# Performance work log

Hardware: AMD Instinct MI355X
Metric: run time of the kernel (lower is better)

Reference implementation:

```python
import jax, jax.numpy as jnp
import numpy as np

N, E, D, T, R, H = 100000, 800000, 128, 4, 4, 8
DK = D // H
LN_EPS = 1e-5


def _per_type_proj(x, W, b, node_type):
    # x:[N,D], W:[T,D,D], b:[T,D] -> select projection by each node's type
    proj = jnp.einsum('ni,tio->nto', x, W) + b[None]          # [N,T,D]
    return jnp.take_along_axis(proj, node_type[:, None, None], axis=1)[:, 0]  # [N,D]


def setup_inputs() -> dict:
    key = jax.random.key(0)
    ks = jax.random.split(key, 12)
    sW = 1.0 / np.sqrt(D)
    sR = np.sqrt(2.0 / (DK + DK))  # glorot for [dk,dk]
    return {
        'x': jax.random.normal(ks[0], (N, D), jnp.float32),
        'node_type': jax.random.randint(ks[1], (N,), 0, T, jnp.int32),
        'edge_index': jax.random.randint(ks[2], (2, E), 0, N, jnp.int32),
        'edge_type': jax.random.randint(ks[3], (E,), 0, R, jnp.int32),
        'edge_spatial': jnp.zeros((E,), jnp.int32),
        'Wk': jax.random.normal(ks[4], (T, D, D), jnp.float32) * sW,
        'bk': jnp.zeros((T, D), jnp.float32),
        'Wq': jax.random.normal(ks[5], (T, D, D), jnp.float32) * sW,
        'bq': jnp.zeros((T, D), jnp.float32),
        'Wv': jax.random.normal(ks[6], (T, D, D), jnp.float32) * sW,
        'bv': jnp.zeros((T, D), jnp.float32),
        'Wa': jax.random.normal(ks[7], (T, D, D), jnp.float32) * sW,
        'ba': jnp.zeros((T, D), jnp.float32),
        'rel_pri': jnp.ones((R, H), jnp.float32),
        'rel_att': jax.random.normal(ks[8], (R, H, DK, DK), jnp.float32) * sR,
        'rel_msg': jax.random.normal(ks[9], (R, H, DK, DK), jnp.float32) * sR,
        'skip': jnp.ones((T,), jnp.float32),
        'ln_gamma': jnp.ones((T, D), jnp.float32),
        'ln_beta': jnp.zeros((T, D), jnp.float32),
    }


def reference(x, node_type, edge_index, edge_type, edge_spatial,
              Wk, bk, Wq, bq, Wv, bv, Wa, ba,
              rel_pri, rel_att, rel_msg, skip, ln_gamma, ln_beta):
    src, dst = edge_index[0], edge_index[1]  # PyG: row0 = source j, row1 = target i

    # per-type linear projections, selected by node type
    K = _per_type_proj(x, Wk, bk, node_type)
    Q = _per_type_proj(x, Wq, bq, node_type)
    V = _per_type_proj(x, Wv, bv, node_type)

    q_e = Q[dst].reshape(E, H, DK)
    k_e = K[src].reshape(E, H, DK)
    v_e = V[src].reshape(E, H, DK)

    # per-relation transforms without materializing [E,H,DK,DK] gathers
    k_rel = jnp.zeros_like(k_e)
    msg = jnp.zeros_like(v_e)
    for r in range(R):
        m = (edge_type == r)[:, None, None]
        k_rel = k_rel + jnp.where(m, jnp.einsum('ehd,hdk->ehk', k_e, rel_att[r]), 0.0)
        msg = msg + jnp.where(m, jnp.einsum('ehd,hdk->ehk', v_e, rel_msg[r]), 0.0)

    logits = (q_e * k_rel).sum(-1) * rel_pri[edge_type] / np.sqrt(DK)  # [E,H]

    # segment softmax over destination nodes
    seg_max = jax.ops.segment_max(logits, dst, num_segments=N)
    seg_max = jnp.where(jnp.isfinite(seg_max), seg_max, 0.0)
    ex = jnp.exp(logits - seg_max[dst])
    denom = jax.ops.segment_sum(ex, dst, num_segments=N)
    att = ex / denom[dst]  # [E,H]

    aggr = jax.ops.segment_sum(msg * att[:, :, None], dst, num_segments=N)  # [N,H,DK]
    h = jax.nn.gelu(aggr.reshape(N, D), approximate=False)

    trans = _per_type_proj(h, Wa, ba, node_type)
    alpha = jax.nn.sigmoid(skip)[node_type][:, None]
    pre = trans * alpha + x * (1.0 - alpha)

    # per-type LayerNorm
    mu = pre.mean(-1, keepdims=True)
    var = ((pre - mu) ** 2).mean(-1, keepdims=True)
    norm = (pre - mu) * jax.lax.rsqrt(var + LN_EPS)
    return norm * ln_gamma[node_type] + ln_beta[node_type]
```

## Files before the change

kernel.cpp:

```cpp
#include <hip/hip_runtime.h>
#include <math.h>

#define D_DIM 128

using bf16x8 = __attribute__((ext_vector_type(8))) short;
using f32x4  = __attribute__((ext_vector_type(4))) float;

__device__ __forceinline__ unsigned short f2bf(float f) {
    unsigned u = __float_as_uint(f);
    u += 0x7fffu + ((u >> 16) & 1u);
    return (unsigned short)(u >> 16);
}

__global__ __launch_bounds__(256)
void count_types_k(const int* __restrict__ nt, int* __restrict__ blockcnt, int N) {
    __shared__ int wcnt[4][4];
    int tid = threadIdx.x;
    int i = blockIdx.x * 256 + tid;
    int w = tid >> 6, l = tid & 63;
    int t = (i < N) ? nt[i] : -1;
    #pragma unroll
    for (int tt = 0; tt < 4; ++tt) {
        unsigned long long m = __ballot(t == tt);
        if (l == 0) wcnt[w][tt] = __popcll(m);
    }
    __syncthreads();
    if (tid < 4) {
        blockcnt[blockIdx.x * 4 + tid] =
            wcnt[0][tid] + wcnt[1][tid] + wcnt[2][tid] + wcnt[3][tid];
    }
}

__global__ __launch_bounds__(256)
void scan_blocks_k(const int* __restrict__ blockcnt, int nb,
                   int* __restrict__ boff, int* __restrict__ pad_off) {
    __shared__ int tot_s[4];
    __shared__ int po_s[5];
    int tid = threadIdx.x;
    int t = tid >> 6, l = tid & 63;
    int sum = 0;
    for (int base = 0; base < nb; base += 64) {
        int b = base + l;
        sum += (b < nb) ? blockcnt[b * 4 + t] : 0;
    }
    #pragma unroll
    for (int m = 1; m < 64; m <<= 1) sum += __shfl_xor(sum, m);
    if (l == 0) tot_s[t] = sum;
    __syncthreads();
    if (tid == 0) {
        int s = 0;
        for (int tt = 0; tt < 4; ++tt) { po_s[tt] = s; s += ((tot_s[tt] + 63) >> 6) << 6; }
        po_s[4] = s;
        for (int tt = 0; tt < 5; ++tt) pad_off[tt] = po_s[tt];
    }
    __syncthreads();
    int run = po_s[t];
    for (int base = 0; base < nb; base += 64) {
        int b = base + l;
        int v = (b < nb) ? blockcnt[b * 4 + t] : 0;
        int incl = v;
        #pragma unroll
        for (int off = 1; off < 64; off <<= 1) {
            int up = __shfl_up(incl, off);
            if (l >= off) incl += up;
        }
        if (b < nb) boff[b * 4 + t] = run + incl - v;
        run += __shfl(incl, 63);
    }
}

__global__ __launch_bounds__(256)
void scatter_types_k(const int* __restrict__ nt, const int* __restrict__ boff,
                     int* __restrict__ order_p, int N) {
    __shared__ int wbase[4][4];
    int tid = threadIdx.x;
    int i = blockIdx.x * 256 + tid;
    int w = tid >> 6, l = tid & 63;
    int t = (i < N) ? nt[i] : -1;
    int rank = 0;
    #pragma unroll
    for (int tt = 0; tt < 4; ++tt) {
        unsigned long long m = __ballot(t == tt);
        if (l == 0) wbase[w][tt] = __popcll(m);
        if (t == tt) rank = __popcll(m & ((1ull << l) - 1ull));
    }
    __syncthreads();
    if (tid < 4) {
        int run = 0;
        for (int ww = 0; ww < 4; ++ww) { int c = wbase[ww][tid]; wbase[ww][tid] = run; run += c; }
    }
    __syncthreads();
    if (i < N) order_p[boff[blockIdx.x * 4 + t] + wbase[w][t] + rank] = i;
}

__global__ void convw_k(const float* __restrict__ Wq, const float* __restrict__ Wa,
                        unsigned short* __restrict__ Wqt, unsigned short* __restrict__ Wat) {
    int i = blockIdx.x * 256 + threadIdx.x;
    int t = i >> 14, rem = i & 16383, row = rem >> 7, col = rem & 127;
    int d = (t << 14) | (col << 7) | row;
    Wqt[d] = f2bf(Wq[i]);
    Wat[d] = f2bf(Wa[i]);
}

__global__ void combine_kr_k(const float* __restrict__ Wk, const float* __restrict__ rel_att,
                             const float* __restrict__ rel_pri,
                             unsigned short* __restrict__ W_kr_t) {
    int idx = blockIdx.x * 256 + threadIdx.x;
    int i = idx & 127;
    int col = (idx >> 7) & 127;
    int r = (idx >> 14) & 3;
    int t = idx >> 16;
    int h = col >> 4, k = col & 15;
    const float* wk = Wk + t * 16384 + i * 128 + h * 16;
    const float* ra = rel_att + ((r * 8 + h) * 16) * 16 + k;
    float s = 0.f;
    #pragma unroll
    for (int d = 0; d < 16; ++d) s += wk[d] * ra[d * 16];
    W_kr_t[idx] = f2bf(s * rel_pri[r * 8 + h] * 0.25f);
}
__global__ void combine_bkr_k(const float* __restrict__ bk, const float* __restrict__ rel_att,
                              const float* __restrict__ rel_pri, float* __restrict__ bkr) {
    int idx = blockIdx.x * 256 + threadIdx.x;
    if (idx >= 2048) return;
    int col = idx & 127;
    int r = (idx >> 7) & 3;
    int t = idx >> 9;
    int h = col >> 4, k = col & 15;
    float s = 0.f;
    #pragma unroll
    for (int d = 0; d < 16; ++d)
        s += bk[t * 128 + h * 16 + d] * rel_att[((r * 8 + h) * 16 + d) * 16 + k];
    bkr[idx] = s * rel_pri[r * 8 + h] * 0.25f;
}

__global__ void combine_vm_k(const float* __restrict__ Wv, const float* __restrict__ rel_msg,
                             unsigned short* __restrict__ W_vm_t) {
    int idx = blockIdx.x * 256 + threadIdx.x;
    int i = idx & 127;
    int col = (idx >> 7) & 127;
    int r = (idx >> 14) & 3;
    int t = idx >> 16;
    int h = col >> 4, k = col & 15;
    const float* wv = Wv + t * 16384 + i * 128 + h * 16;
    const float* rm = rel_msg + ((r * 8 + h) * 16) * 16 + k;
    float s = 0.f;
    #pragma unroll
    for (int d = 0; d < 16; ++d) s += wv[d] * rm[d * 16];
    W_vm_t[idx] = f2bf(s);
}
__global__ void combine_bvm_k(const float* __restrict__ bv, const float* __restrict__ rel_msg,
                              float* __restrict__ bvm) {
    int idx = blockIdx.x * 256 + threadIdx.x;
    if (idx >= 2048) return;
    int col = idx & 127;
    int r = (idx >> 7) & 3;
    int t = idx >> 9;
    int h = col >> 4, k = col & 15;
    float s = 0.f;
    #pragma unroll
    for (int d = 0; d < 16; ++d)
        s += bv[t * 128 + h * 16 + d] * rel_msg[((r * 8 + h) * 16 + d) * 16 + k];
    bvm[idx] = s;
}

__global__ void deg_k(const int* __restrict__ ei, int* __restrict__ deg, int E) {
    int e = blockIdx.x * 256 + threadIdx.x;
    if (e < E) atomicAdd(&deg[ei[E + e]], 1);
}
__global__ void scan1_k(const int* __restrict__ deg, int* __restrict__ excl,
                        int* __restrict__ bsum, int N) {
    __shared__ int s[512];
    int i = blockIdx.x * 512 + threadIdx.x;
    int v = (i < N) ? deg[i] : 0;
    s[threadIdx.x] = v;
    __syncthreads();
    for (int off = 1; off < 512; off <<= 1) {
        int t = (threadIdx.x >= off) ? s[threadIdx.x - off] : 0;
        __syncthreads();
        s[threadIdx.x] += t;
        __syncthreads();
    }
    if (i < N) excl[i] = s[threadIdx.x] - v;
    if (threadIdx.x == 511) bsum[blockIdx.x] = s[511];
}
__global__ void scan2_k(int* __restrict__ bsum, int nb) {
    int l = threadIdx.x & 63;
    int run = 0;
    for (int base = 0; base < nb; base += 64) {
        int b = base + l;
        int v = (b < nb) ? bsum[b] : 0;
        int incl = v;
        #pragma unroll
        for (int off = 1; off < 64; off <<= 1) {
            int up = __shfl_up(incl, off);
            if (l >= off) incl += up;
        }
        if (b < nb) bsum[b] = run + incl - v;
        run += __shfl(incl, 63);
    }
}
__global__ void scan3_k(int* __restrict__ excl, const int* __restrict__ bsum, int N) {
    int i = blockIdx.x * 512 + threadIdx.x;
    if (i < N) excl[i] += bsum[blockIdx.x];
}
__global__ void scatter_edges_k(const int* __restrict__ ei, const int* __restrict__ et,
                                const int* __restrict__ off, int* __restrict__ cursor,
                                int* __restrict__ elist, int E) {
    int e = blockIdx.x * 256 + threadIdx.x;
    if (e < E) {
        int dst = ei[E + e];
        int p = off[dst] + atomicAdd(&cursor[dst], 1);
        elist[p] = (ei[e] << 2) | et[e];
    }
}

__global__ __launch_bounds__(256, 4)
void proj_mfma(const float* __restrict__ x, const int* __restrict__ order_p,
               const int* __restrict__ pad_off,
               const unsigned short* __restrict__ Wqt, const float* __restrict__ bq,
               const unsigned short* __restrict__ W_kr_t, const float* __restrict__ bkr,
               const unsigned short* __restrict__ W_vm_t, const float* __restrict__ bvm,
               unsigned short* __restrict__ Qb, unsigned short* __restrict__ KRb,
               unsigned short* __restrict__ VMb, int N) {
    __shared__ unsigned shmem[64 * 128];
    __shared__ int gid_s[64];
    unsigned* xs = shmem;
    char* stageb = (char*)shmem;
    int tid = threadIdx.x;
    int base = blockIdx.x * 64;
    int t = (base >= pad_off[1]) + (base >= pad_off[2]) + (base >= pad_off[3]);

    if (tid < 64) gid_s[tid] = order_p[base + tid];
    __syncthreads();

    {
        int row = tid >> 2, q = tid & 3;
        int g = gid_s[row];
        const float4* xr = (const float4*)(x + (size_t)(g < 0 ? 0 : g) * 128 + q * 32);
        int swz = (row & 7) << 4;
        #pragma unroll
        for (int v4 = 0; v4 < 8; ++v4) {
            float4 f = (g >= 0) ? xr[v4] : make_float4(0.f, 0.f, 0.f, 0.f);
            unsigned ua = (unsigned)f2bf(f.x) | ((unsigned)f2bf(f.y) << 16);
            unsigned ub = (unsigned)f2bf(f.z) | ((unsigned)f2bf(f.w) << 16);
            int c2 = (q * 16 + v4 * 2) * 4;
            xs[(row << 6) + (((c2) ^ swz) >> 2)] = ua;
            xs[(row << 6) + (((c2 + 4) ^ swz) >> 2)] = ub;
        }
    }
    __syncthreads();

    int w = tid >> 6, l = tid & 63;
    int lr = l & 15, lg = l >> 4;

    bf16x8 afr[4][4];
    #pragma unroll
    for (int j = 0; j < 4; ++j) {
        int row = j * 16 + lr;
        #pragma unroll
        for (int ks = 0; ks < 4; ++ks) {
            int byteoff = (ks * 64 + lg * 16) ^ ((lr & 7) << 4);
            afr[j][ks] = *reinterpret_cast<const bf16x8*>(
                reinterpret_cast<const char*>(&xs[row << 6]) + byteoff);
        }
    }
    __syncthreads();

    #pragma unroll 1
    for (int pass = 0; pass < 4; ++pass) {
        int m0 = (pass & 1) * 2;
        const unsigned short* Wp;
        const float* bp;
        unsigned short* dstp;
        if (pass < 2) { Wp = W_kr_t; bp = bkr; dstp = KRb; }
        else          { Wp = W_vm_t; bp = bvm; dstp = VMb; }
        Wp += (size_t)(t * 4 + m0) << 14;
        bp += (t * 4 + m0) * 128;

        #pragma unroll
        for (int ci = 0; ci < 2; ++ci) {
            int c = w * 2 + ci;
            #pragma unroll
            for (int mm = 0; mm < 2; ++mm) {
                const unsigned short* wb = Wp + ((size_t)mm << 14)
                                         + (size_t)(c * 16 + lr) * 128 + lg * 8;
                bf16x8 wfr[4];
                #pragma unroll
                for (int ks = 0; ks < 4; ++ks) wfr[ks] = *(const bf16x8*)(wb + ks * 32);
                f32x4 acc0 = {0.f,0.f,0.f,0.f}, acc1 = {0.f,0.f,0.f,0.f};
                f32x4 acc2 = {0.f,0.f,0.f,0.f}, acc3 = {0.f,0.f,0.f,0.f};
                #pragma unroll
                for (int ks = 0; ks < 4; ++ks) {
                    acc0 = __builtin_amdgcn_mfma_f32_16x16x32_bf16(wfr[ks], afr[0][ks], acc0, 0, 0, 0);
                    acc1 = __builtin_amdgcn_mfma_f32_16x16x32_bf16(wfr[ks], afr[1][ks], acc1, 0, 0, 0);
                    acc2 = __builtin_amdgcn_mfma_f32_16x16x32_bf16(wfr[ks], afr[2][ks], acc2, 0, 0, 0);
                    acc3 = __builtin_amdgcn_mfma_f32_16x16x32_bf16(wfr[ks], afr[3][ks], acc3, 0, 0, 0);
                }
                float4 bb = *(const float4*)&bp[mm * 128 + c * 16 + lg * 4];
                int colb = (mm * 128 + c * 16 + lg * 4) * 2;
                f32x4 accs[4] = {acc0, acc1, acc2, acc3};
                #pragma unroll
                for (int j = 0; j < 4; ++j) {
                    int node = j * 16 + lr;
                    unsigned p0 = (unsigned)f2bf(accs[j][0] + bb.x) | ((unsigned)f2bf(accs[j][1] + bb.y) << 16);
                    unsigned p1 = (unsigned)f2bf(accs[j][2] + bb.z) | ((unsigned)f2bf(accs[j][3] + bb.w) << 16);
                    int byte = (node * 512 + colb) ^ ((node & 7) << 4);
                    *(uint2*)(stageb + byte) = make_uint2(p0, p1);
                }
            }
        }
        __syncthreads();
        #pragma unroll
        for (int i = 0; i < 8; ++i) {
            int row = w * 16 + i * 2 + (l >> 5);
            int l32 = l & 31;
            int byte = (row * 512 + l32 * 16) ^ ((row & 7) << 4);
            uint4 v = *(const uint4*)(stageb + byte);
            int g = gid_s[row];
            if (g >= 0)
                *(uint4*)&dstp[(size_t)g * 512 + (pass & 1) * 256 + l32 * 8] = v;
        }
        __syncthreads();
    }

    #pragma unroll
    for (int ci = 0; ci < 2; ++ci) {
        int c = w * 2 + ci;
        const unsigned short* wb = Wqt + ((size_t)t << 14) + (size_t)(c * 16 + lr) * 128 + lg * 8;
        bf16x8 wfr[4];
        #pragma unroll
        for (int ks = 0; ks < 4; ++ks) wfr[ks] = *(const bf16x8*)(wb + ks * 32);
        f32x4 acc0 = {0.f,0.f,0.f,0.f}, acc1 = {0.f,0.f,0.f,0.f};
        f32x4 acc2 = {0.f,0.f,0.f,0.f}, acc3 = {0.f,0.f,0.f,0.f};
        #pragma unroll
        for (int ks = 0; ks < 4; ++ks) {
            acc0 = __builtin_amdgcn_mfma_f32_16x16x32_bf16(wfr[ks], afr[0][ks], acc0, 0, 0, 0);
            acc1 = __builtin_amdgcn_mfma_f32_16x16x32_bf16(wfr[ks], afr[1][ks], acc1, 0, 0, 0);
            acc2 = __builtin_amdgcn_mfma_f32_16x16x32_bf16(wfr[ks], afr[2][ks], acc2, 0, 0, 0);
            acc3 = __builtin_amdgcn_mfma_f32_16x16x32_bf16(wfr[ks], afr[3][ks], acc3, 0, 0, 0);
        }
        float4 bb = *(const float4*)&bq[t * 128 + c * 16 + lg * 4];
        int colb = (c * 16 + lg * 4) * 2;
        f32x4 accs[4] = {acc0, acc1, acc2, acc3};
        #pragma unroll
        for (int j = 0; j < 4; ++j) {
            int node = j * 16 + lr;
            unsigned p0 = (unsigned)f2bf(accs[j][0] + bb.x) | ((unsigned)f2bf(accs[j][1] + bb.y) << 16);
            unsigned p1 = (unsigned)f2bf(accs[j][2] + bb.z) | ((unsigned)f2bf(accs[j][3] + bb.w) << 16);
            int byte = (node * 256 + colb) ^ ((node & 7) << 4);
            *(uint2*)(stageb + byte) = make_uint2(p0, p1);
        }
    }
    __syncthreads();
    #pragma unroll
    for (int i = 0; i < 4; ++i) {
        int row = w * 16 + i * 4 + (l >> 4);
        int l16 = l & 15;
        int byte = (row * 256 + l16 * 16) ^ ((row & 7) << 4);
        uint4 v = *(const uint4*)(stageb + byte);
        int g = gid_s[row];
        if (g >= 0) *(uint4*)&Qb[(size_t)g * 128 + l16 * 8] = v;
    }
}

__global__ __launch_bounds__(256)
void edge_fused(const unsigned short* __restrict__ Qb,
                const unsigned short* __restrict__ KRb,
                const unsigned short* __restrict__ VMb,
                const int* __restrict__ off, const int* __restrict__ elist,
                float* __restrict__ aggr, int N, int E) {
    int w = threadIdx.x >> 6, l = threadIdx.x & 63;
    int dst = blockIdx.x * 4 + w;
    if (dst >= N) return;
    int q = l >> 4, c = l & 15;

    float Qf[8];
    {
        bf16x8 qv = *(const bf16x8*)&Qb[(size_t)dst * 128 + c * 8];
        const unsigned* qu = (const unsigned*)&qv;
        #pragma unroll
        for (int i = 0; i < 4; ++i) {
            Qf[2 * i]     = __uint_as_float(qu[i] << 16);
            Qf[2 * i + 1] = __uint_as_float(qu[i] & 0xffff0000u);
        }
    }

    float S[8] = {0.f, 0.f, 0.f, 0.f, 0.f, 0.f, 0.f, 0.f};
    float den = 0.f;

    int e0 = off[dst];
    int e1 = (dst == N - 1) ? E : off[dst + 1];
    int deg = e1 - e0;

    for (int base = 0; base < deg; base += 64) {
        int cnt = min(64, deg - base);
        int pk_l = elist[e0 + min(base + l, deg - 1)];
        for (int s = 0; s < cnt; s += 8) {
            int eA = min(s + q, cnt - 1);
            int eB = min(s + 4 + q, cnt - 1);
            int pkA = __shfl(pk_l, eA);
            int pkB = __shfl(pk_l, eB);
            bf16x8 krA = *(const bf16x8*)&KRb[(size_t)pkA * 128 + c * 8];
            bf16x8 krB = *(const bf16x8*)&KRb[(size_t)pkB * 128 + c * 8];
            bf16x8 vmA = *(const bf16x8*)&VMb[(size_t)pkA * 128 + c * 8];
            bf16x8 vmB = *(const bf16x8*)&VMb[(size_t)pkB * 128 + c * 8];

            const unsigned* ka = (const unsigned*)&krA;
            const unsigned* kb = (const unsigned*)&krB;
            float dtA = 0.f, dtB = 0.f;
            #pragma unroll
            for (int i = 0; i < 4; ++i) {
                dtA = fmaf(Qf[2*i],   __uint_as_float(ka[i] << 16), dtA);
                dtA = fmaf(Qf[2*i+1], __uint_as_float(ka[i] & 0xffff0000u), dtA);
                dtB = fmaf(Qf[2*i],   __uint_as_float(kb[i] << 16), dtB);
                dtB = fmaf(Qf[2*i+1], __uint_as_float(kb[i] & 0xffff0000u), dtB);
            }
            dtA += __shfl_xor(dtA, 1);
            dtB += __shfl_xor(dtB, 1);
            float wA = (s + q < cnt) ? __expf(dtA) : 0.f;
            float wB = (s + 4 + q < cnt) ? __expf(dtB) : 0.f;
            den += wA + wB;

            const unsigned* va = (const unsigned*)&vmA;
            const unsigned* vb = (const unsigned*)&vmB;
            #pragma unroll
            for (int i = 0; i < 4; ++i) {
                S[2*i]   = fmaf(wA, __uint_as_float(va[i] << 16), S[2*i]);
                S[2*i+1] = fmaf(wA, __uint_as_float(va[i] & 0xffff0000u), S[2*i+1]);
                S[2*i]   = fmaf(wB, __uint_as_float(vb[i] << 16), S[2*i]);
                S[2*i+1] = fmaf(wB, __uint_as_float(vb[i] & 0xffff0000u), S[2*i+1]);
            }
        }
    }

    #pragma unroll
    for (int m = 16; m <= 32; m <<= 1) {
        den += __shfl_xor(den, m);
        #pragma unroll
        for (int i = 0; i < 8; ++i) S[i] += __shfl_xor(S[i], m);
    }
    if (q == 0) {
        float inv = (den > 0.f) ? 1.f / den : 0.f;
        float4 o0 = make_float4(S[0]*inv, S[1]*inv, S[2]*inv, S[3]*inv);
        float4 o1 = make_float4(S[4]*inv, S[5]*inv, S[6]*inv, S[7]*inv);
        *(float4*)&aggr[(size_t)dst * 128 + c * 8]     = o0;
        *(float4*)&aggr[(size_t)dst * 128 + c * 8 + 4] = o1;
    }
}

__global__ __launch_bounds__(256)
void node_out_mfma(const float* __restrict__ aggr, const float* __restrict__ x,
                   const int* __restrict__ order_p, const int* __restrict__ pad_off,
                   const unsigned short* __restrict__ Wat, const float* __restrict__ ba,
                   const float* __restrict__ skip, const float* __restrict__ gamma,
                   const float* __restrict__ beta, float* __restrict__ out, int N) {
    __shared__ unsigned hsm[64 * 64];
    __shared__ int gid_s[64];
    int tid = threadIdx.x;
    int base = blockIdx.x * 64;
    int t = (base >= pad_off[1]) + (base >= pad_off[2]) + (base >= pad_off[3]);

    if (tid < 64) gid_s[tid] = order_p[base + tid];
    __syncthreads();

    {
        int row = tid >> 2, q = tid & 3;
        int g = gid_s[row];
        const float4* ar = (const float4*)(aggr + (size_t)(g < 0 ? 0 : g) * 128 + q * 32);
        int swz = (row & 7) << 4;
        #pragma unroll
        for (int v4 = 0; v4 < 8; ++v4) {
            float4 f = (g >= 0) ? ar[v4] : make_float4(0.f, 0.f, 0.f, 0.f);
            float g0 = 0.5f * f.x * (1.f + erff(f.x * 0.70710678118654752f));
            float g1 = 0.5f * f.y * (1.f + erff(f.y * 0.70710678118654752f));
            float g2 = 0.5f * f.z * (1.f + erff(f.z * 0.70710678118654752f));
            float g3 = 0.5f * f.w * (1.f + erff(f.w * 0.70710678118654752f));
            unsigned ua = (unsigned)f2bf(g0) | ((unsigned)f2bf(g1) << 16);
            unsigned ub = (unsigned)f2bf(g2) | ((unsigned)f2bf(g3) << 16);
            int c2 = (q * 16 + v4 * 2) * 4;
            hsm[(row << 6) + (((c2) ^ swz) >> 2)] = ua;
            hsm[(row << 6) + (((c2 + 4) ^ swz) >> 2)] = ub;
        }
    }
    __syncthreads();

    int w = tid >> 6, l = tid & 63;
    int rowbase = w * 16, lr = l & 15, lg = l >> 4;
    int myrow = rowbase + lr;

    bf16x8 afr[4];
    #pragma unroll
    for (int ks = 0; ks < 4; ++ks) {
        int byteoff = (ks * 64 + lg * 16) ^ ((lr & 7) << 4);
        afr[ks] = *reinterpret_cast<const bf16x8*>(
            reinterpret_cast<const char*>(&hsm[myrow << 6]) + byteoff);
    }

    float al = 1.f / (1.f + __expf(-skip[t]));
    int g = gid_s[myrow];

    float pre[8][4];
    float s = 0.f, sq = 0.f;

    #pragma unroll
    for (int c = 0; c < 8; ++c) {
        const unsigned short* wb = Wat + ((size_t)t << 14) + (size_t)(c * 16 + lr) * 128 + lg * 8;
        f32x4 acc = {0.f, 0.f, 0.f, 0.f};
        #pragma unroll
        for (int ks = 0; ks < 4; ++ks)
            acc = __builtin_amdgcn_mfma_f32_16x16x32_bf16(
                *(const bf16x8*)(wb + ks * 32), afr[ks], acc, 0, 0, 0);
        float4 bav = *(const float4*)&ba[t * 128 + c * 16 + lg * 4];
        float4 xv = (g >= 0) ? *(const float4*)&x[(size_t)g * 128 + c * 16 + lg * 4]
                             : make_float4(0.f, 0.f, 0.f, 0.f);
        float p0 = (acc[0] + bav.x) * al + xv.x * (1.f - al);
        float p1 = (acc[1] + bav.y) * al + xv.y * (1.f - al);
        float p2 = (acc[2] + bav.z) * al + xv.z * (1.f - al);
        float p3 = (acc[3] + bav.w) * al + xv.w * (1.f - al);
        pre[c][0] = p0; pre[c][1] = p1; pre[c][2] = p2; pre[c][3] = p3;
        s += p0 + p1 + p2 + p3;
        sq += p0 * p0 + p1 * p1 + p2 * p2 + p3 * p3;
    }

    s  += __shfl_xor(s, 16);  sq += __shfl_xor(sq, 16);
    s  += __shfl_xor(s, 32);  sq += __shfl_xor(sq, 32);
    float mu = s * (1.f / 128.f);
    float var = sq * (1.f / 128.f) - mu * mu;
    float rs = rsqrtf(fmaxf(var, 0.f) + 1e-5f);

    #pragma unroll
    for (int c = 0; c < 8; ++c) {
        float4 ga = *(const float4*)&gamma[t * 128 + c * 16 + lg * 4];
        float4 be = *(const float4*)&beta[t * 128 + c * 16 + lg * 4];
        float4 o;
        o.x = (pre[c][0] - mu) * rs * ga.x + be.x;
        o.y = (pre[c][1] - mu) * rs * ga.y + be.y;
        o.z = (pre[c][2] - mu) * rs * ga.z + be.z;
        o.w = (pre[c][3] - mu) * rs * ga.w + be.w;
        if (g >= 0) *(float4*)&out[(size_t)g * 128 + c * 16 + lg * 4] = o;
    }
}

extern "C" void kernel_launch(void* const* d_in, const int* in_sizes, int n_in,
                              void* d_out, int out_size, void* d_ws, size_t ws_size,
                              hipStream_t stream) {
    const float* x   = (const float*)d_in[0];
    const int*   nt  = (const int*)d_in[1];
    const int*   ei  = (const int*)d_in[2];
    const int*   et  = (const int*)d_in[3];
    const float* Wk = (const float*)d_in[5];  const float* bk = (const float*)d_in[6];
    const float* Wq = (const float*)d_in[7];  const float* bq = (const float*)d_in[8];
    const float* Wv = (const float*)d_in[9];  const float* bv = (const float*)d_in[10];
    const float* Wa = (const float*)d_in[11]; const float* ba = (const float*)d_in[12];
    const float* rel_pri = (const float*)d_in[13];
    const float* rel_att = (const float*)d_in[14];
    const float* rel_msg = (const float*)d_in[15];
    const float* skip    = (const float*)d_in[16];
    const float* gamma   = (const float*)d_in[17];
    const float* beta    = (const float*)d_in[18];

    const int N = in_sizes[0] / 128;
    const int E = in_sizes[3];
    const int NB = (N + 511) / 512;
    const int NB256 = (N + 255) / 256;

    unsigned short* Qb  = (unsigned short*)d_ws;
    unsigned short* KRb = Qb + (size_t)N * 128;
    unsigned short* VMb = KRb + (size_t)N * 512;
    unsigned short* Wqt = VMb + (size_t)N * 512;
    unsigned short* Wat = Wqt + 65536;
    unsigned short* Wkrt = Wat + 65536;
    unsigned short* Wvmt = Wkrt + 262144;
    float* bkr = (float*)(Wvmt + 262144);
    float* bvm = bkr + 2048;
    int* order_p = (int*)(bvm + 2048);
    int* blockcnt = order_p + N + 320;
    int* boff     = blockcnt + NB256 * 4;
    int* pad_off  = boff + NB256 * 4;
    int* deg     = pad_off + 8;
    int* off     = deg + N;
    int* bsum    = off + N;
    int* cursorD = bsum + NB + 8;
    int* elist   = cursorD + N;
    float* aggr  = (float*)d_out;

    hipMemsetAsync(order_p, 0xFF, (size_t)(N + 320) * sizeof(int), stream);
    hipMemsetAsync(deg, 0, (size_t)N * sizeof(int), stream);
    hipMemsetAsync(cursorD, 0, (size_t)N * sizeof(int), stream);

    count_types_k<<<NB256, 256, 0, stream>>>(nt, blockcnt, N);
    scan_blocks_k<<<1, 256, 0, stream>>>(blockcnt, NB256, boff, pad_off);
    scatter_types_k<<<NB256, 256, 0, stream>>>(nt, boff, order_p, N);

    convw_k<<<256, 256, 0, stream>>>(Wq, Wa, Wqt, Wat);
    combine_kr_k<<<1024, 256, 0, stream>>>(Wk, rel_att, rel_pri, Wkrt);
    combine_bkr_k<<<8, 256, 0, stream>>>(bk, rel_att, rel_pri, bkr);
    combine_vm_k<<<1024, 256, 0, stream>>>(Wv, rel_msg, Wvmt);
    combine_bvm_k<<<8, 256, 0, stream>>>(bv, rel_msg, bvm);

    deg_k<<<(E + 255) / 256, 256, 0, stream>>>(ei, deg, E);
    scan1_k<<<NB, 512, 0, stream>>>(deg, off, bsum, N);
    scan2_k<<<1, 64, 0, stream>>>(bsum, NB);
    scan3_k<<<NB, 512, 0, stream>>>(off, bsum, N);
    scatter_edges_k<<<(E + 255) / 256, 256, 0, stream>>>(ei, et, off, cursorD, elist, E);

    int nb64 = (N + 252 + 63) / 64;
    proj_mfma<<<nb64, 256, 0, stream>>>(x, order_p, pad_off, Wqt, bq, Wkrt, bkr, Wvmt, bvm,
                                        Qb, KRb, VMb, N);
    edge_fused<<<(N + 3) / 4, 256, 0, stream>>>(Qb, KRb, VMb, off, elist, aggr, N, E);
    node_out_mfma<<<nb64, 256, 0, stream>>>(aggr, x, order_p, pad_off, Wat, ba, skip,
                                            gamma, beta, (float*)d_out, N);
}
```

Measured before the change: 392.2 us.

## Process two destination nodes per wavefront and merge weight-prep kernels

The edge aggregation kernel now has each wavefront handle two consecutive destination nodes, so it issues twice as many independent gathers and exp/FMA chains per iteration to hide memory latency. The four weight/bias combine kernels and the transpose kernel are merged into one launch. The order_p memset is replaced by clearing only the padding slots inside the scan kernel, and the two zeroing memsets are merged by making deg and cursorD contiguous. In exchange, the edge kernel uses more registers, and when the two nodes have unequal degrees one half of the wavefront does wasted work.

Result: no change. 392.3 us (+0.0%).

```diff
diff --git a/kernel.cpp b/kernel.cpp
--- a/kernel.cpp
+++ b/kernel.cpp
@@ -32,8 +32,9 @@
 }
 
 __global__ __launch_bounds__(256)
-void scan_blocks_k(const int* __restrict__ blockcnt, int nb,
-                   int* __restrict__ boff, int* __restrict__ pad_off) {
+void scan_blocks_k(const int* __restrict__ blockcnt, int nb, int N,
+                   int* __restrict__ boff, int* __restrict__ pad_off,
+                   int* __restrict__ order_p) {
     __shared__ int tot_s[4];
     __shared__ int po_s[5];
     int tid = threadIdx.x;
@@ -53,6 +54,13 @@
         po_s[4] = s;
         for (int tt = 0; tt < 5; ++tt) pad_off[tt] = po_s[tt];
     }
+    __syncthreads();
+    #pragma unroll 1
+    for (int tt = 0; tt < 4; ++tt) {
+        int gs = po_s[tt] + tot_s[tt], ge = po_s[tt + 1];
+        for (int i = gs + tid; i < ge; i += 256) order_p[i] = -1;
+    }
+    for (int i = po_s[4] + tid; i < N + 320; i += 256) order_p[i] = -1;
     __syncthreads();
     int run = po_s[t];
     for (int base = 0; base < nb; base += 64) {
@@ -93,74 +101,58 @@
     if (i < N) order_p[boff[blockIdx.x * 4 + t] + wbase[w][t] + rank] = i;
 }
 
-__global__ void convw_k(const float* __restrict__ Wq, const float* __restrict__ Wa,
-                        unsigned short* __restrict__ Wqt, unsigned short* __restrict__ Wat) {
-    int i = blockIdx.x * 256 + threadIdx.x;
-    int t = i >> 14, rem = i & 16383, row = rem >> 7, col = rem & 127;
-    int d = (t << 14) | (col << 7) | row;
-    Wqt[d] = f2bf(Wq[i]);
-    Wat[d] = f2bf(Wa[i]);
-}
-
-__global__ void combine_kr_k(const float* __restrict__ Wk, const float* __restrict__ rel_att,
-                             const float* __restrict__ rel_pri,
-                             unsigned short* __restrict__ W_kr_t) {
+__global__ __launch_bounds__(256)
+void prep_weights_k(const float* __restrict__ Wk, const float* __restrict__ Wq,
+                    const float* __restrict__ Wv, const float* __restrict__ Wa,
+                    const float* __restrict__ bk, const float* __restrict__ bv,
+                    const float* __restrict__ rel_att, const float* __restrict__ rel_msg,
+                    const float* __restrict__ rel_pri,
+                    unsigned short* __restrict__ Wqt, unsigned short* __restrict__ Wat,
+                    unsigned short* __restrict__ Wkrt, unsigned short* __restrict__ Wvmt,
+                    float* __restrict__ bkr, float* __restrict__ bvm) {
     int idx = blockIdx.x * 256 + threadIdx.x;
     int i = idx & 127;
     int col = (idx >> 7) & 127;
     int r = (idx >> 14) & 3;
     int t = idx >> 16;
     int h = col >> 4, k = col & 15;
-    const float* wk = Wk + t * 16384 + i * 128 + h * 16;
-    const float* ra = rel_att + ((r * 8 + h) * 16) * 16 + k;
-    float s = 0.f;
-    #pragma unroll
-    for (int d = 0; d < 16; ++d) s += wk[d] * ra[d * 16];
-    W_kr_t[idx] = f2bf(s * rel_pri[r * 8 + h] * 0.25f);
-}
-__global__ void combine_bkr_k(const float* __restrict__ bk, const float* __restrict__ rel_att,
-                              const float* __restrict__ rel_pri, float* __restrict__ bkr) {
-    int idx = blockIdx.x * 256 + threadIdx.x;
-    if (idx >= 2048) return;
-    int col = idx & 127;
-    int r = (idx >> 7) & 3;
-    int t = idx >> 9;
-    int h = col >> 4, k = col & 15;
-    float s = 0.f;
-    #pragma unroll
-    for (int d = 0; d < 16; ++d)
-        s += bk[t * 128 + h * 16 + d] * rel_att[((r * 8 + h) * 16 + d) * 16 + k];
-    bkr[idx] = s * rel_pri[r * 8 + h] * 0.25f;
-}
-
-__global__ void combine_vm_k(const float* __restrict__ Wv, const float* __restrict__ rel_msg,
-                             unsigned short* __restrict__ W_vm_t) {
-    int idx = blockIdx.x * 256 + threadIdx.x;
-    int i = idx & 127;
-    int col = (idx >> 7) & 127;
-    int r = (idx >> 14) & 3;
-    int t = idx >> 16;
-    int h = col >> 4, k = col & 15;
-    const float* wv = Wv + t * 16384 + i * 128 + h * 16;
-    const float* rm = rel_msg + ((r * 8 + h) * 16) * 16 + k;
-    float s = 0.f;
-    #pragma unroll
-    for (int d = 0; d < 16; ++d) s += wv[d] * rm[d * 16];
-    W_vm_t[idx] = f2bf(s);
-}
-__global__ void combine_bvm_k(const float* __restrict__ bv, const float* __restrict__ rel_msg,
-                              float* __restrict__ bvm) {
-    int idx = blockIdx.x * 256 + threadIdx.x;
-    if (idx >= 2048) return;
-    int col = idx & 127;
-    int r = (idx >> 7) & 3;
-    int t = idx >> 9;
-    int h = col >> 4, k = col & 15;
-    float s = 0.f;
-    #pragma unroll
-    for (int d = 0; d < 16; ++d)
-        s += bv[t * 128 + h * 16 + d] * rel_msg[((r * 8 + h) * 16 + d) * 16 + k];
-    bvm[idx] = s;
+    {
+        const float* wk = Wk + t * 16384 + i * 128 + h * 16;
+        const float* wv = Wv + t * 16384 + i * 128 + h * 16;
+        const float* ra = rel_att + ((r * 8 + h) * 16) * 16 + k;
+        const float* rm = rel_msg + ((r * 8 + h) * 16) * 16 + k;
+        float s1 = 0.f, s2 = 0.f;
+        #pragma unroll
+        for (int d = 0; d < 16; ++d) {
+            s1 += wk[d] * ra[d * 16];
+            s2 += wv[d] * rm[d * 16];
+        }
+        Wkrt[idx] = f2bf(s1 * rel_pri[r * 8 + h] * 0.25f);
+        Wvmt[idx] = f2bf(s2);
+    }
+    if (idx < 65536) {
+        int t2 = idx >> 14, rem = idx & 16383, row = rem >> 7, col2 = rem & 127;
+        int d = (t2 << 14) | (col2 << 7) | row;
+        Wqt[d] = f2bf(Wq[idx]);
+        Wat[d] = f2bf(Wa[idx]);
+    }
+    if (idx < 4096) {
+        int bi = idx & 2047;
+        int col3 = bi & 127, r3 = (bi >> 7) & 3, t3 = bi >> 9;
+        int h3 = col3 >> 4, k3 = col3 & 15;
+        float s = 0.f;
+        if (idx < 2048) {
+            #pragma unroll
+            for (int d = 0; d < 16; ++d)
+                s += bk[t3 * 128 + h3 * 16 + d] * rel_att[((r3 * 8 + h3) * 16 + d) * 16 + k3];
+            bkr[bi] = s * rel_pri[r3 * 8 + h3] * 0.25f;
+        } else {
+            #pragma unroll
+            for (int d = 0; d < 16; ++d)
+                s += bv[t3 * 128 + h3 * 16 + d] * rel_msg[((r3 * 8 + h3) * 16 + d) * 16 + k3];
+            bvm[bi] = s;
+        }
+    }
 }
 
 __global__ void deg_k(const int* __restrict__ ei, int* __restrict__ deg, int E) {
@@ -370,81 +362,129 @@
                 const int* __restrict__ off, const int* __restrict__ elist,
                 float* __restrict__ aggr, int N, int E) {
     int w = threadIdx.x >> 6, l = threadIdx.x & 63;
-    int dst = blockIdx.x * 4 + w;
-    if (dst >= N) return;
+    int dstA = (blockIdx.x * 4 + w) * 2;
+    if (dstA >= N) return;
+    int dstB = dstA + 1;
+    bool hasB = (dstB < N);
     int q = l >> 4, c = l & 15;
 
-    float Qf[8];
+    float QfA[8], QfB[8];
     {
-        bf16x8 qv = *(const bf16x8*)&Qb[(size_t)dst * 128 + c * 8];
+        bf16x8 qv = *(const bf16x8*)&Qb[(size_t)dstA * 128 + c * 8];
         const unsigned* qu = (const unsigned*)&qv;
         #pragma unroll
         for (int i = 0; i < 4; ++i) {
-            Qf[2 * i]     = __uint_as_float(qu[i] << 16);
-            Qf[2 * i + 1] = __uint_as_float(qu[i] & 0xffff0000u);
-        }
-    }
-
-    float S[8] = {0.f, 0.f, 0.f, 0.f, 0.f, 0.f, 0.f, 0.f};
-    float den = 0.f;
-
-    int e0 = off[dst];
-    int e1 = (dst == N - 1) ? E : off[dst + 1];
-    int deg = e1 - e0;
-
-    for (int base = 0; base < deg; base += 64) {
-        int cnt = min(64, deg - base);
-        int pk_l = elist[e0 + min(base + l, deg - 1)];
-        for (int s = 0; s < cnt; s += 8) {
-            int eA = min(s + q, cnt - 1);
-            int eB = min(s + 4 + q, cnt - 1);
-            int pkA = __shfl(pk_l, eA);
-            int pkB = __shfl(pk_l, eB);
-            bf16x8 krA = *(const bf16x8*)&KRb[(size_t)pkA * 128 + c * 8];
-            bf16x8 krB = *(const bf16x8*)&KRb[(size_t)pkB * 128 + c * 8];
-            bf16x8 vmA = *(const bf16x8*)&VMb[(size_t)pkA * 128 + c * 8];
-            bf16x8 vmB = *(const bf16x8*)&VMb[(size_t)pkB * 128 + c * 8];
-
-            const unsigned* ka = (const unsigned*)&krA;
-            const unsigned* kb = (const unsigned*)&krB;
-            float dtA = 0.f, dtB = 0.f;
+            QfA[2*i]   = __uint_as_float(qu[i] << 16);
+            QfA[2*i+1] = __uint_as_float(qu[i] & 0xffff0000u);
+        }
+    }
+    {
+        bf16x8 qv = *(const bf16x8*)&Qb[(size_t)(hasB ? dstB : dstA) * 128 + c * 8];
+        const unsigned* qu = (const unsigned*)&qv;
+        #pragma unroll
+        for (int i = 0; i < 4; ++i) {
+            QfB[2*i]   = __uint_as_float(qu[i] << 16);
+            QfB[2*i+1] = __uint_as_float(qu[i] & 0xffff0000u);
+        }
+    }
+
+    int eA0 = off[dstA];
+    int eA1 = hasB ? off[dstB] : E;
+    int eB0 = eA1;
+    int eB1 = hasB ? ((dstB == N - 1) ? E : off[dstB + 1]) : eA1;
+    int degA = eA1 - eA0;
+    int degB = eB1 - eB0;
+    int mdeg = max(degA, degB);
+
+    float SA[8] = {0.f,0.f,0.f,0.f,0.f,0.f,0.f,0.f};
+    float SB[8] = {0.f,0.f,0.f,0.f,0.f,0.f,0.f,0.f};
+    float denA = 0.f, denB = 0.f;
+
+    for (int base = 0; base < mdeg; base += 64) {
+        int cntA = min(64, degA - base);
+        int cntB = min(64, degB - base);
+        int pkA_l = (degA > 0) ? elist[eA0 + min(base + l, degA - 1)] : 0;
+        int pkB_l = (degB > 0) ? elist[eB0 + min(base + l, degB - 1)] : 0;
+        int mcnt = max(cntA, cntB);
+        for (int s = 0; s < mcnt; s += 8) {
+            int clA = max(cntA - 1, 0), clB = max(cntB - 1, 0);
+            int pkA0 = __shfl(pkA_l, min(s + q, clA));
+            int pkA1 = __shfl(pkA_l, min(s + 4 + q, clA));
+            int pkB0 = __shfl(pkB_l, min(s + q, clB));
+            int pkB1 = __shfl(pkB_l, min(s + 4 + q, clB));
+            bf16x8 krA0 = *(const bf16x8*)&KRb[(size_t)pkA0 * 128 + c * 8];
+            bf16x8 krA1 = *(const bf16x8*)&KRb[(size_t)pkA1 * 128 + c * 8];
+            bf16x8 krB0 = *(const bf16x8*)&KRb[(size_t)pkB0 * 128 + c * 8];
+            bf16x8 krB1 = *(const bf16x8*)&KRb[(size_t)pkB1 * 128 + c * 8];
+            bf16x8 vmA0 = *(const bf16x8*)&VMb[(size_t)pkA0 * 128 + c * 8];
+            bf16x8 vmA1 = *(const bf16x8*)&VMb[(size_t)pkA1 * 128 + c * 8];
+            bf16x8 vmB0 = *(const bf16x8*)&VMb[(size_t)pkB0 * 128 + c * 8];
+            bf16x8 vmB1 = *(const bf16x8*)&VMb[(size_t)pkB1 * 128 + c * 8];
+
+            const unsigned* ka0 = (const unsigned*)&krA0;
+            const unsigned* ka1 = (const unsigned*)&krA1;
+            const unsigned* kb0 = (const unsigned*)&krB0;
+            const unsigned* kb1 = (const unsigned*)&krB1;
+            float dA0 = 0.f, dA1 = 0.f, dB0 = 0.f, dB1 = 0.f;
             #pragma unroll
             for (int i = 0; i < 4; ++i) {
-                dtA = fmaf(Qf[2*i],   __uint_as_float(ka[i] << 16), dtA);
-                dtA = fmaf(Qf[2*i+1], __uint_as_float(ka[i] & 0xffff0000u), dtA);
-                dtB = fmaf(Qf[2*i],   __uint_as_float(kb[i] << 16), dtB);
-                dtB = fmaf(Qf[2*i+1], __uint_as_float(kb[i] & 0xffff0000u), dtB);
+                dA0 = fmaf(QfA[2*i],   __uint_as_float(ka0[i] << 16), dA0);
+                dA0 = fmaf(QfA[2*i+1], __uint_as_float(ka0[i] & 0xffff0000u), dA0);
+                dA1 = fmaf(QfA[2*i],   __uint_as_float(ka1[i] << 16), dA1);
+                dA1 = fmaf(QfA[2*i+1], __uint_as_float(ka1[i] & 0xffff0000u), dA1);
+                dB0 = fmaf(QfB[2*i],   __uint_as_float(kb0[i] << 16), dB0);
+                dB0 = fmaf(QfB[2*i+1], __uint_as_float(kb0[i] & 0xffff0000u), dB0);
+                dB1 = fmaf(QfB[2*i],   __uint_as_float(kb1[i] << 16), dB1);
+                dB1 = fmaf(QfB[2*i+1], __uint_as_float(kb1[i] & 0xffff0000u), dB1);
             }
-            dtA += __shfl_xor(dtA, 1);
-            dtB += __shfl_xor(dtB, 1);
-            float wA = (s + q < cnt) ? __expf(dtA) : 0.f;
-            float wB = (s + 4 + q < cnt) ? __expf(dtB) : 0.f;
-            den += wA + wB;
-
-            const unsigned* va = (const unsigned*)&vmA;
-            const unsigned* vb = (const unsigned*)&vmB;
+            dA0 += __shfl_xor(dA0, 1);
+            dA1 += __shfl_xor(dA1, 1);
+            dB0 += __shfl_xor(dB0, 1);
+            dB1 += __shfl_xor(dB1, 1);
+            float wA0 = (s + q < cntA)     ? __expf(dA0) : 0.f;
+            float wA1 = (s + 4 + q < cntA) ? __expf(dA1) : 0.f;
+            float wB0 = (s + q < cntB)     ? __expf(dB0) : 0.f;
+            float wB1 = (s + 4 + q < cntB) ? __expf(dB1) : 0.f;
+            denA += wA0 + wA1;
+            denB += wB0 + wB1;
+
+            const unsigned* va0 = (const unsigned*)&vmA0;
+            const unsigned* va1 = (const unsigned*)&vmA1;
+            const unsigned* vb0 = (const unsigned*)&vmB0;
+            const unsigned* vb1 = (const unsigned*)&vmB1;
             #pragma unroll
             for (int i = 0; i < 4; ++i) {
-                S[2*i]   = fmaf(wA, __uint_as_float(va[i] << 16), S[2*i]);
-                S[2*i+1] = fmaf(wA, __uint_as_float(va[i] & 0xffff0000u), S[2*i+1]);
-                S[2*i]   = fmaf(wB, __uint_as_float(vb[i] << 16), S[2*i]);
-                S[2*i+1] = fmaf(wB, __uint_as_float(vb[i] & 0xffff0000u), S[2*i+1]);
+                SA[2*i]   = fmaf(wA0, __uint_as_float(va0[i] << 16), SA[2*i]);
+                SA[2*i+1] = fmaf(wA0, __uint_as_float(va0[i] & 0xffff0000u), SA[2*i+1]);
+                SA[2*i]   = fmaf(wA1, __uint_as_float(va1[i] << 16), SA[2*i]);
+                SA[2*i+1] = fmaf(wA1, __uint_as_float(va1[i] & 0xffff0000u), SA[2*i+1]);
+                SB[2*i]   = fmaf(wB0, __uint_as_float(vb0[i] << 16), SB[2*i]);
+                SB[2*i+1] = fmaf(wB0, __uint_as_float(vb0[i] & 0xffff0000u), SB[2*i+1]);
+                SB[2*i]   = fmaf(wB1, __uint_as_float(vb1[i] << 16), SB[2*i]);
+                SB[2*i+1] = fmaf(wB1, __uint_as_float(vb1[i] & 0xffff0000u), SB[2*i+1]);
             }
         }
     }
 
     #pragma unroll
     for (int m = 16; m <= 32; m <<= 1) {
-        den += __shfl_xor(den, m);
-        #pragma unroll
-        for (int i = 0; i < 8; ++i) S[i] += __shfl_xor(S[i], m);
-    }
-    if (q == 0) {
-        float inv = (den > 0.f) ? 1.f / den : 0.f;
-        float4 o0 = make_float4(S[0]*inv, S[1]*inv, S[2]*inv, S[3]*inv);
-        float4 o1 = make_float4(S[4]*inv, S[5]*inv, S[6]*inv, S[7]*inv);
-        *(float4*)&aggr[(size_t)dst * 128 + c * 8]     = o0;
-        *(float4*)&aggr[(size_t)dst * 128 + c * 8 + 4] = o1;
+        denA += __shfl_xor(denA, m);
+        denB += __shfl_xor(denB, m);
+        #pragma unroll
+        for (int i = 0; i < 8; ++i) {
+            SA[i] += __shfl_xor(SA[i], m);
+            SB[i] += __shfl_xor(SB[i], m);
+        }
+    }
+    float invA = (denA > 0.f) ? 1.f / denA : 0.f;
+    float invB = (denB > 0.f) ? 1.f / denB : 0.f;
+    float o[8];
+    #pragma unroll
+    for (int i = 0; i < 8; ++i) o[i] = (q == 1) ? SB[i] * invB : SA[i] * invA;
+    int sd = (q == 1) ? dstB : dstA;
+    if (q == 0 || (q == 1 && hasB)) {
+        *(float4*)&aggr[(size_t)sd * 128 + c * 8]     = make_float4(o[0], o[1], o[2], o[3]);
+        *(float4*)&aggr[(size_t)sd * 128 + c * 8 + 4] = make_float4(o[4], o[5], o[6], o[7]);
     }
 }
 
@@ -578,25 +618,20 @@
     int* boff     = blockcnt + NB256 * 4;
     int* pad_off  = boff + NB256 * 4;
     int* deg     = pad_off + 8;
-    int* off     = deg + N;
+    int* cursorD = deg + N;
+    int* off     = cursorD + N;
     int* bsum    = off + N;
-    int* cursorD = bsum + NB + 8;
-    int* elist   = cursorD + N;
+    int* elist   = bsum + NB + 8;
     float* aggr  = (float*)d_out;
 
-    hipMemsetAsync(order_p, 0xFF, (size_t)(N + 320) * sizeof(int), stream);
-    hipMemsetAsync(deg, 0, (size_t)N * sizeof(int), stream);
-    hipMemsetAsync(cursorD, 0, (size_t)N * sizeof(int), stream);
+    hipMemsetAsync(deg, 0, (size_t)(2 * N) * sizeof(int), stream);
 
     count_types_k<<<NB256, 256, 0, stream>>>(nt, blockcnt, N);
-    scan_blocks_k<<<1, 256, 0, stream>>>(blockcnt, NB256, boff, pad_off);
+    scan_blocks_k<<<1, 256, 0, stream>>>(blockcnt, NB256, N, boff, pad_off, order_p);
     scatter_types_k<<<NB256, 256, 0, stream>>>(nt, boff, order_p, N);
 
-    convw_k<<<256, 256, 0, stream>>>(Wq, Wa, Wqt, Wat);
-    combine_kr_k<<<1024, 256, 0, stream>>>(Wk, rel_att, rel_pri, Wkrt);
-    combine_bkr_k<<<8, 256, 0, stream>>>(bk, rel_att, rel_pri, bkr);
-    combine_vm_k<<<1024, 256, 0, stream>>>(Wv, rel_msg, Wvmt);
-    combine_bvm_k<<<8, 256, 0, stream>>>(bv, rel_msg, bvm);
+    prep_weights_k<<<1024, 256, 0, stream>>>(Wk, Wq, Wv, Wa, bk, bv, rel_att, rel_msg,
+                                             rel_pri, Wqt, Wat, Wkrt, Wvmt, bkr, bvm);
 
     deg_k<<<(E + 255) / 256, 256, 0, stream>>>(ei, deg, E);
     scan1_k<<<NB, 512, 0, stream>>>(deg, off, bsum, N);
@@ -607,7 +642,8 @@
     int nb64 = (N + 252 + 63) / 64;
     proj_mfma<<<nb64, 256, 0, stream>>>(x, order_p, pad_off, Wqt, bq, Wkrt, bkr, Wvmt, bvm,
                                         Qb, KRb, VMb, N);
-    edge_fused<<<(N + 3) / 4, 256, 0, stream>>>(Qb, KRb, VMb, off, elist, aggr, N, E);
+    int npairs = (N + 1) / 2;
+    edge_fused<<<(npairs + 3) / 4, 256, 0, stream>>>(Qb, KRb, VMb, off, elist, aggr, N, E);
     node_out_mfma<<<nb64, 256, 0, stream>>>(aggr, x, order_p, pad_off, Wat, ba, skip,
                                             gamma, beta, (float*)d_out, N);
 }
```
